# Optimization experiments

Hardware: AMD Instinct MI355X
Metric: run time of the kernel (lower is better)

## Reference

```python
import jax, jax.numpy as jnp
import numpy as np

O, I = 11008, 4096      # out_features, in_features (LLaMA-7B MLP up-proj)
TOKENS = 4096
GS = 64                 # group_size
NG = I // GS            # groups per output row (no padding: I % GS == 0)
B_MAX = 7               # 2**(num_bits-1) - 1 for num_bits=4


def setup_inputs() -> dict:
    key = jax.random.key(0)
    k1, k2, k3 = jax.random.split(key, 3)
    x = jax.random.normal(k1, (TOKENS, I), dtype=jnp.float32)
    w = jax.random.normal(k2, (O, I), dtype=jnp.float32) * 0.02
    bias = jax.random.normal(k3, (O,), dtype=jnp.float32) * 0.01
    # --- group-wise asymmetric 4-bit quantization (compress, num_bits=4, symmetric=False) ---
    g = w.reshape(O, NG, GS)
    mn = jnp.min(g, axis=2, keepdims=True)                       # [O, NG, 1]
    mx = jnp.max(g, axis=2, keepdims=True)
    scale = B_MAX / (mx - mn)
    q = jnp.clip(jnp.round((g - mn) * scale), 0, B_MAX).astype(jnp.uint8)
    # pack: first half of group -> high nibble, second half -> low nibble
    packed = ((q[:, :, : GS // 2] << 4) | q[:, :, GS // 2 :]).astype(jnp.uint8)  # [O, NG, GS//2]
    inv_scale = (1.0 / scale).astype(jnp.float32)                # [O, NG, 1]
    return {"x": x, "packed": packed, "mn": mn, "inv_scale": inv_scale, "bias": bias}


def reference(x, packed, mn, inv_scale, bias):
    # decompress: unpack nibbles, dequantize, then F.linear
    hi = (packed >> 4).astype(x.dtype)        # group positions [0, GS//2)
    lo = (packed & 0x0F).astype(x.dtype)      # group positions [GS//2, GS)
    q = jnp.concatenate([hi, lo], axis=2)     # [O, NG, GS]
    w = (q * inv_scale + mn).reshape(O, I)    # dequantized weight [O, I]
    return x @ w.T + bias                     # [TOKENS, O]
```

## Files before the change

kernel.cpp:

```cpp
#include <hip/hip_runtime.h>
#include <hip/hip_fp16.h>
#include <stdint.h>

#define TOKENS 4096
#define OFEAT  11008
#define IFEAT  4096
#define NGRP   64
#define NGTOT  (OFEAT*NGRP)

#define BM 128
#define BN 128
#define BK 32
#define NT_M (TOKENS/BM)
#define NT_N (OFEAT/BN)
#define NWG  (NT_M*NT_N)

typedef _Float16 half8 __attribute__((ext_vector_type(8)));
typedef float    floatx4 __attribute__((ext_vector_type(4)));

#define AS1 __attribute__((address_space(1)))
#define AS3 __attribute__((address_space(3)))

__device__ __forceinline__ void gload_lds16(const void* g, void* l) {
  __builtin_amdgcn_global_load_lds((const AS1 uint32_t*)g, (AS3 uint32_t*)l, 16, 0, 0);
}

__global__ __launch_bounds__(256) void cvt_x(const float* __restrict__ x,
                                             _Float16* __restrict__ xh) {
  int t = blockIdx.x * 256 + threadIdx.x;
  const float4* x4 = (const float4*)x;
  float4 a = x4[2*t], c = x4[2*t + 1];
  half8 h;
  h[0] = (_Float16)a.x; h[1] = (_Float16)a.y; h[2] = (_Float16)a.z; h[3] = (_Float16)a.w;
  h[4] = (_Float16)c.x; h[5] = (_Float16)c.y; h[6] = (_Float16)c.z; h[7] = (_Float16)c.w;
  *(half8*)(xh + (size_t)t * 8) = h;
}

__global__ __launch_bounds__(256) void dequant_w(const void* __restrict__ packed,
                                                 const float* __restrict__ mn,
                                                 const float* __restrict__ inv_scale,
                                                 _Float16* __restrict__ W) {
  int t = blockIdx.x * 256 + threadIdx.x;
  int g = t >> 3;
  int s = t & 7;

  __shared__ int is_i32_s;
  if (threadIdx.x == 0) {
    const int* pi = (const int*)packed;
    int ok = 1;
#pragma unroll
    for (int i = 0; i < 8; ++i) ok &= ((unsigned)pi[i] < 256u);
    is_i32_s = ok;
  }
  __syncthreads();

  const int hi = (s < 4) ? 1 : 0;
  const int bbase = (s & 3) * 8;
  unsigned char b[8];
  if (is_i32_s) {
    const int4* p = (const int4*)packed + ((size_t)g * 32 + bbase) / 4;
    int4 w0 = p[0], w1 = p[1];
    b[0] = (unsigned char)w0.x; b[1] = (unsigned char)w0.y;
    b[2] = (unsigned char)w0.z; b[3] = (unsigned char)w0.w;
    b[4] = (unsigned char)w1.x; b[5] = (unsigned char)w1.y;
    b[6] = (unsigned char)w1.z; b[7] = (unsigned char)w1.w;
  } else {
    const unsigned char* p8 = (const unsigned char*)packed + (size_t)g * 32 + bbase;
    uint2 w = *(const uint2*)p8;
    b[0] = w.x & 0xff; b[1] = (w.x >> 8) & 0xff; b[2] = (w.x >> 16) & 0xff; b[3] = (w.x >> 24) & 0xff;
    b[4] = w.y & 0xff; b[5] = (w.y >> 8) & 0xff; b[6] = (w.y >> 16) & 0xff; b[7] = (w.y >> 24) & 0xff;
  }

  float m  = mn[g];
  float sc = inv_scale[g];
  int shift = hi ? 4 : 0;
  half8 h;
#pragma unroll
  for (int j = 0; j < 8; ++j) {
    unsigned q = (b[j] >> shift) & 0xF;
    h[j] = (_Float16)fmaf((float)q, sc, m);
  }
  size_t off = (size_t)g * 64 + (hi ? 0 : 32) + (s & 3) * 8;
  *(half8*)(W + off) = h;
}

__global__ __launch_bounds__(256) void gemm_f16(const _Float16* __restrict__ A,
                                                const _Float16* __restrict__ B,
                                                const float* __restrict__ bias,
                                                float* __restrict__ C) {
  __shared__ _Float16 sA[BM * BK];
  __shared__ _Float16 sB[BN * BK];

  int bid = blockIdx.x;
  int swz = (bid & 7) * (NWG >> 3) + (bid >> 3);
  int tm = swz / NT_N, tn = swz % NT_N;

  int tid  = threadIdx.x;
  int wave = tid >> 6, lane = tid & 63;
  int wr = (wave >> 1) * 64;
  int wc = (wave & 1) * 64;

  const size_t K2 = (size_t)IFEAT * 2;
  int row0 = tid >> 2;
  int kb0  = (tid & 3) << 4;
  const char* gA = (const char*)A + (size_t)(tm * BM + row0) * K2 + kb0;
  const char* gB = (const char*)B + (size_t)(tn * BN + row0) * K2 + kb0;
  char* lA = (char*)sA + wave * 1024;
  char* lB = (char*)sB + wave * 1024;

  floatx4 acc[4][4] = {};

  int lr = lane & 15;
  int lk = (lane >> 4) << 3;
  const _Float16* sAr = &sA[(wr + lr) * BK + lk];
  const _Float16* sBr = &sB[(wc + lr) * BK + lk];

  for (int kt = 0; kt < IFEAT / BK; ++kt) {
    gload_lds16(gA,           lA);
    gload_lds16(gA + 64 * K2, lA + 4096);
    gload_lds16(gB,           lB);
    gload_lds16(gB + 64 * K2, lB + 4096);
    gA += BK * 2; gB += BK * 2;
    __syncthreads();

    half8 af[4], bf[4];
#pragma unroll
    for (int i = 0; i < 4; ++i) af[i] = *(const half8*)(sAr + i * 16 * BK);
#pragma unroll
    for (int j = 0; j < 4; ++j) bf[j] = *(const half8*)(sBr + j * 16 * BK);
#pragma unroll
    for (int i = 0; i < 4; ++i)
#pragma unroll
      for (int j = 0; j < 4; ++j)
        acc[i][j] = __builtin_amdgcn_mfma_f32_16x16x32_f16(af[i], bf[j], acc[i][j], 0, 0, 0);
    __syncthreads();
  }

  int lq = (lane >> 4) << 2;
#pragma unroll
  for (int j = 0; j < 4; ++j) {
    int col = tn * BN + wc + j * 16 + lr;
    float bv = bias[col];
#pragma unroll
    for (int i = 0; i < 4; ++i) {
      int row = tm * BM + wr + i * 16 + lq;
#pragma unroll
      for (int p = 0; p < 4; ++p) {
        C[(size_t)(row + p) * OFEAT + col] = acc[i][j][p] + bv;
      }
    }
  }
}

extern "C" void kernel_launch(void* const* d_in, const int* in_sizes, int n_in,
                              void* d_out, int out_size, void* d_ws, size_t ws_size,
                              hipStream_t stream) {
  const float* x         = (const float*)d_in[0];
  const void*  packed    = d_in[1];
  const float* mn        = (const float*)d_in[2];
  const float* inv_scale = (const float*)d_in[3];
  const float* bias      = (const float*)d_in[4];
  float* out = (float*)d_out;

  _Float16* xh = (_Float16*)d_ws;
  _Float16* wh = (_Float16*)((char*)d_ws + (size_t)TOKENS * IFEAT * 2);

  cvt_x<<<(TOKENS * IFEAT) / (256 * 8), 256, 0, stream>>>(x, xh);
  dequant_w<<<(NGTOT * 8) / 256, 256, 0, stream>>>(packed, mn, inv_scale, wh);
  gemm_f16<<<NWG, 256, 0, stream>>>(xh, wh, bias, out);
}
```

Baseline: 750.9 us.

## Enlarge GEMM tiles to 256x256 with triple-buffered swizzled LDS pipeline

The f16 GEMM now uses 256x256 output tiles and 512 threads, each wave computing a 128x64 sub-tile. It replaces the two-barrier-per-step loop with a three-stage LDS ring: direct global-to-LDS loads for tile k+2 are issued while tile k is computed, and explicit vmcnt waits plus one barrier sit between stages. An XOR swizzle on the K chunk offset aims to avoid LDS bank conflicts, and s_setprio is raised around the MFMA block. The goal is to hide global-load latency and raise arithmetic intensity per LDS byte, at the cost of more registers per thread (a 32-accumulator array), 96KB of LDS, and fewer workgroups in flight.

Result: faster. 648.9 us (-13.6%).

```diff
diff --git a/kernel.cpp b/kernel.cpp
--- a/kernel.cpp
+++ b/kernel.cpp
@@ -8,12 +8,13 @@
 #define NGRP   64
 #define NGTOT  (OFEAT*NGRP)
 
-#define BM 128
-#define BN 128
+#define BM 256
+#define BN 256
 #define BK 32
 #define NT_M (TOKENS/BM)
 #define NT_N (OFEAT/BN)
 #define NWG  (NT_M*NT_N)
+#define NKT  (IFEAT/BK)
 
 typedef _Float16 half8 __attribute__((ext_vector_type(8)));
 typedef float    floatx4 __attribute__((ext_vector_type(4)));
@@ -21,7 +22,7 @@
 #define AS1 __attribute__((address_space(1)))
 #define AS3 __attribute__((address_space(3)))
 
-__device__ __forceinline__ void gload_lds16(const void* g, void* l) {
+__device__ __forceinline__ void gload16(const void* g, void* l) {
   __builtin_amdgcn_global_load_lds((const AS1 uint32_t*)g, (AS3 uint32_t*)l, 16, 0, 0);
 }
 
@@ -84,12 +85,42 @@
   *(half8*)(W + off) = h;
 }
 
-__global__ __launch_bounds__(256) void gemm_f16(const _Float16* __restrict__ A,
-                                                const _Float16* __restrict__ B,
-                                                const float* __restrict__ bias,
-                                                float* __restrict__ C) {
-  __shared__ _Float16 sA[BM * BK];
-  __shared__ _Float16 sB[BN * BK];
+
+__device__ __forceinline__ void stage_tile(const char* a, const char* b,
+                                           char* lA, char* lB, size_t K2) {
+  gload16(a,            lA);
+  gload16(a + 128 * K2, lA + 8192);
+  gload16(b,            lB);
+  gload16(b + 128 * K2, lB + 8192);
+}
+
+__device__ __forceinline__ void compute_tile(const _Float16* bA, const _Float16* bB,
+                                             floatx4 (&acc)[8][4],
+                                             int lofs, int arow, int brow) {
+  half8 af[8], bf[4];
+#pragma unroll
+  for (int fr = 0; fr < 8; ++fr)
+    af[fr] = *(const half8*)(bA + (arow + fr * 16) * 32 + lofs);
+#pragma unroll
+  for (int fc = 0; fc < 4; ++fc)
+    bf[fc] = *(const half8*)(bB + (brow + fc * 16) * 32 + lofs);
+  __builtin_amdgcn_s_setprio(1);
+#pragma unroll
+  for (int fr = 0; fr < 8; ++fr)
+#pragma unroll
+    for (int fc = 0; fc < 4; ++fc)
+      acc[fr][fc] = __builtin_amdgcn_mfma_f32_16x16x32_f16(af[fr], bf[fc], acc[fr][fc], 0, 0, 0);
+  __builtin_amdgcn_s_setprio(0);
+}
+
+#define WAITBAR4() asm volatile("s_waitcnt vmcnt(4)\n\ts_barrier" ::: "memory")
+#define WAITBAR0() asm volatile("s_waitcnt vmcnt(0)\n\ts_barrier" ::: "memory")
+
+__global__ __launch_bounds__(512, 2) void gemm_f16(const _Float16* __restrict__ A,
+                                                   const _Float16* __restrict__ B,
+                                                   const float* __restrict__ bias,
+                                                   float* __restrict__ C) {
+  __shared__ __align__(16) _Float16 smem[3 * 16384];
 
   int bid = blockIdx.x;
   int swz = (bid & 7) * (NWG >> 3) + (bid >> 3);
@@ -97,57 +128,64 @@
 
   int tid  = threadIdx.x;
   int wave = tid >> 6, lane = tid & 63;
-  int wr = (wave >> 1) * 64;
-  int wc = (wave & 1) * 64;
+  int wm = wave >> 2, wn = wave & 3;
 
   const size_t K2 = (size_t)IFEAT * 2;
-  int row0 = tid >> 2;
-  int kb0  = (tid & 3) << 4;
-  const char* gA = (const char*)A + (size_t)(tm * BM + row0) * K2 + kb0;
-  const char* gB = (const char*)B + (size_t)(tn * BN + row0) * K2 + kb0;
-  char* lA = (char*)sA + wave * 1024;
-  char* lB = (char*)sB + wave * 1024;
-
-  floatx4 acc[4][4] = {};
-
-  int lr = lane & 15;
-  int lk = (lane >> 4) << 3;
-  const _Float16* sAr = &sA[(wr + lr) * BK + lk];
-  const _Float16* sBr = &sB[(wc + lr) * BK + lk];
-
-  for (int kt = 0; kt < IFEAT / BK; ++kt) {
-    gload_lds16(gA,           lA);
-    gload_lds16(gA + 64 * K2, lA + 4096);
-    gload_lds16(gB,           lB);
-    gload_lds16(gB + 64 * K2, lB + 4096);
-    gA += BK * 2; gB += BK * 2;
-    __syncthreads();
-
-    half8 af[4], bf[4];
-#pragma unroll
-    for (int i = 0; i < 4; ++i) af[i] = *(const half8*)(sAr + i * 16 * BK);
-#pragma unroll
-    for (int j = 0; j < 4; ++j) bf[j] = *(const half8*)(sBr + j * 16 * BK);
-#pragma unroll
-    for (int i = 0; i < 4; ++i)
-#pragma unroll
-      for (int j = 0; j < 4; ++j)
-        acc[i][j] = __builtin_amdgcn_mfma_f32_16x16x32_f16(af[i], bf[j], acc[i][j], 0, 0, 0);
-    __syncthreads();
-  }
-
-  int lq = (lane >> 4) << 2;
-#pragma unroll
-  for (int j = 0; j < 4; ++j) {
-    int col = tn * BN + wc + j * 16 + lr;
+  int kswz = (((tid & 3) ^ ((tid >> 3) & 3)) << 4);
+  const char* gA = (const char*)A + (size_t)(tm * BM + (tid >> 2)) * K2 + kswz;
+  const char* gB = (const char*)B + (size_t)(tn * BN + (tid >> 2)) * K2 + kswz;
+
+  int dstoff = wave * 1024;
+  _Float16* A0 = smem;              _Float16* B0 = smem + 8192;
+  _Float16* A1 = smem + 16384;      _Float16* B1 = smem + 24576;
+  _Float16* A2 = smem + 32768;      _Float16* B2 = smem + 40960;
+  char* lA0 = (char*)A0 + dstoff;  char* lB0 = (char*)B0 + dstoff;
+  char* lA1 = (char*)A1 + dstoff;  char* lB1 = (char*)B1 + dstoff;
+  char* lA2 = (char*)A2 + dstoff;  char* lB2 = (char*)B2 + dstoff;
+
+  int x = lane & 15;
+  int pslot = (lane >> 4) ^ ((x >> 1) & 3);
+  int lofs = x * 32 + pslot * 8;
+  const int arow = wm * 128;
+  const int brow = wn * 64;
+
+  floatx4 acc[8][4] = {};
+
+  stage_tile(gA,      gB,      lA0, lB0, K2);
+  stage_tile(gA + 64, gB + 64, lA1, lB1, K2);
+  WAITBAR4();
+
+  for (int t = 0; t < NKT - 2; t += 3) {
+    const char* a = gA + (size_t)(t + 2) * 64;
+    const char* b = gB + (size_t)(t + 2) * 64;
+    stage_tile(a, b, lA2, lB2, K2);
+    compute_tile(A0, B0, acc, lofs, arow, brow);
+    WAITBAR4();
+
+    stage_tile(a + 64, b + 64, lA0, lB0, K2);
+    compute_tile(A1, B1, acc, lofs, arow, brow);
+    WAITBAR4();
+
+    stage_tile(a + 128, b + 128, lA1, lB1, K2);
+    compute_tile(A2, B2, acc, lofs, arow, brow);
+    WAITBAR4();
+  }
+  compute_tile(A0, B0, acc, lofs, arow, brow);
+  WAITBAR0();
+  compute_tile(A1, B1, acc, lofs, arow, brow);
+
+  int rowq = (lane >> 4) << 2;
+  int colbase = tn * BN + brow + x;
+#pragma unroll
+  for (int fc = 0; fc < 4; ++fc) {
+    int col = colbase + fc * 16;
     float bv = bias[col];
 #pragma unroll
-    for (int i = 0; i < 4; ++i) {
-      int row = tm * BM + wr + i * 16 + lq;
-#pragma unroll
-      for (int p = 0; p < 4; ++p) {
-        C[(size_t)(row + p) * OFEAT + col] = acc[i][j][p] + bv;
-      }
+    for (int fr = 0; fr < 8; ++fr) {
+      int row = tm * BM + arow + fr * 16 + rowq;
+#pragma unroll
+      for (int p = 0; p < 4; ++p)
+        C[(size_t)(row + p) * OFEAT + col] = acc[fr][fc][p] + bv;
     }
   }
 }
@@ -167,5 +205,5 @@
 
   cvt_x<<<(TOKENS * IFEAT) / (256 * 8), 256, 0, stream>>>(x, xh);
   dequant_w<<<(NGTOT * 8) / 256, 256, 0, stream>>>(packed, mn, inv_scale, wh);
-  gemm_f16<<<NWG, 256, 0, stream>>>(xh, wh, bias, out);
-}
+  gemm_f16<<<NWG, 512, 0, stream>>>(xh, wh, bias, out);
+}
```
